# Kernel optimization log

Measured on AMD Instinct MI355X. Metric: run time of the kernel, lower is better.

The kernel has to match this reference:

```python
import jax, jax.numpy as jnp
import numpy as np

N_NODES = 50000
N_EDGES = 1000000
D = 64
L = 3
BN_EPS = 1e-5


def setup_inputs() -> dict:
    key = jax.random.key(0)
    ks = jax.random.split(key, 6)
    x = jax.random.normal(ks[0], (N_NODES, D), dtype=jnp.float32)
    edge_src = jax.random.randint(ks[1], (N_EDGES,), 0, N_NODES)
    edge_dst = jax.random.randint(ks[2], (N_EDGES,), 0, N_NODES)
    edge_weight = jax.random.uniform(ks[3], (N_EDGES,), dtype=jnp.float32)
    W = jax.random.normal(ks[4], (L, D, D), dtype=jnp.float32) * (1.0 / np.sqrt(D))
    b = jnp.zeros((L, D), dtype=jnp.float32)
    prelu_a = jnp.full((L,), 0.25, dtype=jnp.float32)  # torch PReLU default init
    bn_gamma = jnp.ones((L, D), dtype=jnp.float32)
    bn_beta = jnp.zeros((L, D), dtype=jnp.float32)
    return {"x": x, "edge_src": edge_src, "edge_dst": edge_dst,
            "edge_weight": edge_weight, "W": W, "b": b, "prelu_a": prelu_a,
            "bn_gamma": bn_gamma, "bn_beta": bn_beta}


def reference(x, edge_src, edge_dst, edge_weight, W, b, prelu_a, bn_gamma, bn_beta):
    n = x.shape[0]
    h = x
    for i in range(L):
        h_in = h
        # GCNConv (normalize=False): aggregate edge_weight * (h @ W)[src] at dst, + bias
        xw = h @ W[i]                                       # [N, D]
        msg = edge_weight[:, None] * xw[edge_src]            # [E, D] gather
        agg = jax.ops.segment_sum(msg, edge_dst, num_segments=n) + b[i]
        # PReLU (single shared parameter per module)
        h = jnp.where(agg >= 0, agg, prelu_a[i] * agg)
        if i > 0:
            h = h + h_in
        # BatchNorm1d, training-mode batch statistics over nodes
        mean = jnp.mean(h, axis=0)
        var = jnp.mean((h - mean) ** 2, axis=0)  # biased variance, as torch BN
        h = bn_gamma[i] * (h - mean) * jax.lax.rsqrt(var + BN_EPS) + bn_beta[i]
        # dropout p=0.0 -> identity
    return h
```

## Files before the change

kernel.cpp:

```cpp
#include <hip/hip_runtime.h>
#include <hip/hip_fp16.h>

#define N_NODES 50000
#define N_EDGES 1000000
#define D 64
#define L 3
#define BN_EPS 1e-5f
#define NB_SCAN ((N_NODES + 255) / 256)
#define AGG_BLOCKS ((N_NODES + 31) / 32)
#define NXCD 8
#define BN_XSTRIDE (L * 2 * D)

__device__ inline int get_xcc() {
    int x;
    asm volatile("s_getreg_b32 %0, hwreg(HW_REG_XCC_ID)" : "=s"(x));
    return x & (NXCD - 1);
}

__device__ inline void bn_affine8(const float* __restrict__ bnsum_l,
                                  const float* __restrict__ gamma,
                                  const float* __restrict__ beta,
                                  int c, float& sc, float& sh) {
    float s1 = 0.f, s2 = 0.f;
#pragma unroll
    for (int x = 0; x < NXCD; x++) {
        s1 += bnsum_l[(size_t)x * BN_XSTRIDE + c];
        s2 += bnsum_l[(size_t)x * BN_XSTRIDE + D + c];
    }
    float mean = s1 * (1.f / N_NODES);
    float var = fmaf(-mean, mean, s2 * (1.f / N_NODES));
    float inv = rsqrtf(var + BN_EPS);
    sc = gamma[c] * inv;
    sh = fmaf(-mean, sc, beta[c]);
}

__device__ inline float unpack_w(unsigned int m) {
    __half_raw hr;
    hr.x = (unsigned short)(m & 0xffffu);
    __half h = *reinterpret_cast<__half*>(&hr);
    return __half2float(h);
}

__device__ inline float2 unpack_x2(unsigned int q) {
    __half2 h2 = *reinterpret_cast<__half2*>(&q);
    return __half22float2(h2);
}

__device__ inline float2 ntload_f2(const float2* p) {
    unsigned long long u = __builtin_nontemporal_load((const unsigned long long*)p);
    float2 r;
    r.x = __uint_as_float((unsigned int)(u & 0xffffffffull));
    r.y = __uint_as_float((unsigned int)(u >> 32));
    return r;
}

__device__ inline void ntstore_f2(float2* p, float2 v) {
    unsigned long long u =
        ((unsigned long long)__float_as_uint(v.y) << 32) | (unsigned long long)__float_as_uint(v.x);
    __builtin_nontemporal_store(u, (unsigned long long*)p);
}

__global__ void init_kernel(int* __restrict__ counts8, float* __restrict__ bnsum8) {
    int i = blockIdx.x * blockDim.x + threadIdx.x;
    int stride = gridDim.x * blockDim.x;
    for (int j = i; j < NXCD * N_NODES; j += stride) counts8[j] = 0;
    for (int j = i; j < NXCD * BN_XSTRIDE; j += stride) bnsum8[j] = 0.f;
}

__global__ void count_kernel(const int* __restrict__ dst, int* __restrict__ counts8,
                             unsigned short* __restrict__ rankx) {
    int xcd = get_xcc();
    int* mycnt = counts8 + (size_t)xcd * N_NODES;
    int i = blockIdx.x * blockDim.x + threadIdx.x;
    int stride = gridDim.x * blockDim.x;
    for (int e = i; e < N_EDGES; e += stride) {
        int r = atomicAdd(&mycnt[dst[e]], 1);
        rankx[e] = (unsigned short)(r | (xcd << 13));
    }
}

__global__ __launch_bounds__(256) void scanA_kernel(const int* __restrict__ counts8,
                                                    int* __restrict__ counts,
                                                    int* __restrict__ blocksum) {
    __shared__ int buf[256];
    int t = threadIdx.x, b = blockIdx.x;
    int i = b * 256 + t;
    int v = 0;
    if (i < N_NODES) {
#pragma unroll
        for (int x = 0; x < NXCD; x++) v += counts8[(size_t)x * N_NODES + i];
        counts[i] = v;
    }
    buf[t] = v;
    __syncthreads();
    for (int off = 128; off > 0; off >>= 1) {
        if (t < off) buf[t] += buf[t + off];
        __syncthreads();
    }
    if (t == 0) blocksum[b] = buf[0];
}

__global__ __launch_bounds__(256) void scanB_kernel(const int* __restrict__ blocksum,
                                                    int* __restrict__ blockoff,
                                                    int* __restrict__ row_ptr) {
    __shared__ int buf[256];
    int t = threadIdx.x;
    int v = (t < NB_SCAN) ? blocksum[t] : 0;
    buf[t] = v;
    __syncthreads();
    for (int off = 1; off < 256; off <<= 1) {
        int u = (t >= off) ? buf[t - off] : 0;
        __syncthreads();
        buf[t] += u;
        __syncthreads();
    }
    if (t < NB_SCAN) blockoff[t] = buf[t] - v;
    if (t == NB_SCAN - 1) row_ptr[N_NODES] = buf[t];
}

__global__ __launch_bounds__(256) void scanC_kernel(const int* __restrict__ counts,
                                                    const int* __restrict__ counts8,
                                                    const int* __restrict__ blockoff,
                                                    int* __restrict__ row_ptr,
                                                    int* __restrict__ offs8) {
    __shared__ int buf[256];
    int t = threadIdx.x, b = blockIdx.x;
    int i = b * 256 + t;
    int v = (i < N_NODES) ? counts[i] : 0;
    buf[t] = v;
    __syncthreads();
    for (int off = 1; off < 256; off <<= 1) {
        int u = (t >= off) ? buf[t - off] : 0;
        __syncthreads();
        buf[t] += u;
        __syncthreads();
    }
    if (i < N_NODES) {
        int base = blockoff[b] + buf[t] - v;
        row_ptr[i] = base;
#pragma unroll
        for (int x = 0; x < NXCD; x++) {
            offs8[(size_t)x * N_NODES + i] = base;
            base += counts8[(size_t)x * N_NODES + i];
        }
    }
}

__global__ void fill_kernel(const int* __restrict__ src, const int* __restrict__ dst,
                            const float* __restrict__ w,
                            const unsigned short* __restrict__ rankx,
                            const int* __restrict__ offs8,
                            unsigned int* __restrict__ em) {
    int i = blockIdx.x * blockDim.x + threadIdx.x;
    int stride = gridDim.x * blockDim.x;
    for (int e = i; e < N_EDGES; e += stride) {
        int d = dst[e];
        unsigned rx = rankx[e];
        int p = offs8[(size_t)(rx >> 13) * N_NODES + d] + (int)(rx & 0x1fffu);
        __half h = __float2half_rn(w[e]);
        unsigned short wb = reinterpret_cast<__half_raw*>(&h)->x;
        em[p] = ((unsigned int)src[e] << 16) | (unsigned int)wb;
    }
}

__global__ __launch_bounds__(256) void gemm_kernel(const float* __restrict__ hraw,
                                                   const float* __restrict__ bnsum_p,
                                                   const float* __restrict__ gamma_p,
                                                   const float* __restrict__ beta_p,
                                                   const float* __restrict__ Wl,
                                                   __half* __restrict__ xw) {
    __shared__ float aff[2][D];
    int tid = threadIdx.x, lane = tid & 63, wave = tid >> 6;
    if (tid < D) {
        float sc = 1.f, sh = 0.f;
        if (bnsum_p) bn_affine8(bnsum_p, gamma_p, beta_p, tid, sc, sh);
        aff[0][tid] = sc;
        aff[1][tid] = sh;
    }
    __syncthreads();
    float Wreg[D];
    float biasc = 0.f;
#pragma unroll
    for (int k = 0; k < D; k++) {
        float wkc = Wl[k * D + lane];
        biasc = fmaf(aff[1][k], wkc, biasc);
        Wreg[k] = wkc * aff[0][k];
    }
    int gw = blockIdx.x * 4 + wave, nw = gridDim.x * 4;
    for (int v = gw; v < N_NODES; v += nw) {
        const float* hp = hraw + (size_t)__builtin_amdgcn_readfirstlane(v) * D;
        float acc = biasc;
#pragma unroll
        for (int k = 0; k < D; k++) acc = fmaf(hp[k], Wreg[k], acc);
        xw[v * D + lane] = __float2half_rn(acc);
    }
}

__global__ __launch_bounds__(256) void agg_kernel(const uint2* __restrict__ xw,
                                                  const int* __restrict__ row_ptr,
                                                  const unsigned int* __restrict__ em,
                                                  const float* __restrict__ bl,
                                                  const float* __restrict__ pa,
                                                  const float* __restrict__ hraw_prev,
                                                  const float* __restrict__ bnsum_p,
                                                  const float* __restrict__ gamma_p,
                                                  const float* __restrict__ beta_p,
                                                  float* __restrict__ hpre,
                                                  float* __restrict__ bnsum_l) {
    __shared__ float r1[D], r2[D];
    int tid = threadIdx.x, lane = tid & 63;
    int sub = tid >> 4;
    int fl = lane & 15;
    int srcbase = lane & 48;
    if (tid < D) { r1[tid] = 0.f; r2[tid] = 0.f; }
    __syncthreads();

    float al = pa[0];
    int c0 = 4 * fl;
    float4 bias = ((const float4*)bl)[fl];
    float sc0 = 0, sc1 = 0, sc2 = 0, sc3 = 0, sh0 = 0, sh1 = 0, sh2 = 0, sh3 = 0;
    if (hraw_prev) {
        bn_affine8(bnsum_p, gamma_p, beta_p, c0 + 0, sc0, sh0);
        bn_affine8(bnsum_p, gamma_p, beta_p, c0 + 1, sc1, sh1);
        bn_affine8(bnsum_p, gamma_p, beta_p, c0 + 2, sc2, sh2);
        bn_affine8(bnsum_p, gamma_p, beta_p, c0 + 3, sc3, sh3);
    }
    float t1_0 = 0, t1_1 = 0, t1_2 = 0, t1_3 = 0;
    float t2_0 = 0, t2_1 = 0, t2_2 = 0, t2_3 = 0;

    int v0 = (blockIdx.x * 16 + sub) * 2;
    if (v0 < N_NODES) {
        int2 e01 = *(const int2*)(row_ptr + v0);
        int e0 = e01.x, m = e01.y;
        int e2 = row_ptr[v0 + 2];
        float A0 = 0, A1 = 0, A2 = 0, A3 = 0, B0 = 0, B1 = 0, B2 = 0, B3 = 0;
        unsigned mo = (e0 + fl < e2) ? __builtin_nontemporal_load(em + e0 + fl) : 0u;
        for (int e = e0; e < e2; e += 16) {
            unsigned mo_nx =
                (e + 16 + fl < e2) ? __builtin_nontemporal_load(em + e + 16 + fl) : 0u;
            unsigned mj[16];
            uint2 q[16];
#pragma unroll
            for (int j = 0; j < 16; j++) {
                mj[j] = (unsigned)__shfl((int)mo, srcbase + j, 64);
                q[j] = xw[(mj[j] >> 16) * 16 + fl];
            }
#pragma unroll
            for (int j = 0; j < 16; j++) {
                float w = unpack_w(mj[j]);
                bool isB = (e + j) >= m;
                float wa = isB ? 0.f : w;
                float wb = isB ? w : 0.f;
                float2 f01 = unpack_x2(q[j].x);
                float2 f23 = unpack_x2(q[j].y);
                A0 = fmaf(wa, f01.x, A0); A1 = fmaf(wa, f01.y, A1);
                A2 = fmaf(wa, f23.x, A2); A3 = fmaf(wa, f23.y, A3);
                B0 = fmaf(wb, f01.x, B0); B1 = fmaf(wb, f01.y, B1);
                B2 = fmaf(wb, f23.x, B2); B3 = fmaf(wb, f23.y, B3);
            }
            mo = mo_nx;
        }
#pragma unroll
        for (int n = 0; n < 2; n++) {
            int v = v0 + n;
            float h0 = (n ? B0 : A0) + bias.x;
            float h1 = (n ? B1 : A1) + bias.y;
            float h2 = (n ? B2 : A2) + bias.z;
            float h3 = (n ? B3 : A3) + bias.w;
            h0 = h0 >= 0.f ? h0 : al * h0;
            h1 = h1 >= 0.f ? h1 : al * h1;
            h2 = h2 >= 0.f ? h2 : al * h2;
            h3 = h3 >= 0.f ? h3 : al * h3;
            if (hraw_prev) {
                float2 p01 = ntload_f2((const float2*)hraw_prev + v * 32 + 2 * fl);
                float2 p23 = ntload_f2((const float2*)hraw_prev + v * 32 + 2 * fl + 1);
                h0 = fmaf(p01.x, sc0, h0 + sh0);
                h1 = fmaf(p01.y, sc1, h1 + sh1);
                h2 = fmaf(p23.x, sc2, h2 + sh2);
                h3 = fmaf(p23.y, sc3, h3 + sh3);
            }
            ntstore_f2((float2*)hpre + v * 32 + 2 * fl, make_float2(h0, h1));
            ntstore_f2((float2*)hpre + v * 32 + 2 * fl + 1, make_float2(h2, h3));
            t1_0 += h0; t1_1 += h1; t1_2 += h2; t1_3 += h3;
            t2_0 = fmaf(h0, h0, t2_0);
            t2_1 = fmaf(h1, h1, t2_1);
            t2_2 = fmaf(h2, h2, t2_2);
            t2_3 = fmaf(h3, h3, t2_3);
        }
    }
    t1_0 += __shfl_xor(t1_0, 16, 64); t1_0 += __shfl_xor(t1_0, 32, 64);
    t1_1 += __shfl_xor(t1_1, 16, 64); t1_1 += __shfl_xor(t1_1, 32, 64);
    t1_2 += __shfl_xor(t1_2, 16, 64); t1_2 += __shfl_xor(t1_2, 32, 64);
    t1_3 += __shfl_xor(t1_3, 16, 64); t1_3 += __shfl_xor(t1_3, 32, 64);
    t2_0 += __shfl_xor(t2_0, 16, 64); t2_0 += __shfl_xor(t2_0, 32, 64);
    t2_1 += __shfl_xor(t2_1, 16, 64); t2_1 += __shfl_xor(t2_1, 32, 64);
    t2_2 += __shfl_xor(t2_2, 16, 64); t2_2 += __shfl_xor(t2_2, 32, 64);
    t2_3 += __shfl_xor(t2_3, 16, 64); t2_3 += __shfl_xor(t2_3, 32, 64);
    if (lane < 16) {
        atomicAdd(&r1[c0 + 0], t1_0);
        atomicAdd(&r1[c0 + 1], t1_1);
        atomicAdd(&r1[c0 + 2], t1_2);
        atomicAdd(&r1[c0 + 3], t1_3);
        atomicAdd(&r2[c0 + 0], t2_0);
        atomicAdd(&r2[c0 + 1], t2_1);
        atomicAdd(&r2[c0 + 2], t2_2);
        atomicAdd(&r2[c0 + 3], t2_3);
    }
    __syncthreads();
    if (tid < D) {
        float* myb = bnsum_l + (size_t)get_xcc() * BN_XSTRIDE;
        atomicAdd(&myb[tid], r1[tid]);
        atomicAdd(&myb[D + tid], r2[tid]);
    }
}

__global__ __launch_bounds__(256) void bnapply_kernel(const float* __restrict__ hpre,
                                                      const float* __restrict__ bnsum_p,
                                                      const float* __restrict__ gamma_p,
                                                      const float* __restrict__ beta_p,
                                                      float* __restrict__ out) {
    __shared__ float aff[2][D];
    int tid = threadIdx.x;
    if (tid < D) {
        float sc, sh;
        bn_affine8(bnsum_p, gamma_p, beta_p, tid, sc, sh);
        aff[0][tid] = sc;
        aff[1][tid] = sh;
    }
    __syncthreads();
    int i = blockIdx.x * blockDim.x + tid;
    int stride = gridDim.x * blockDim.x;
    const int NQ = N_NODES * D / 4;
    for (int j = i; j < NQ; j += stride) {
        float4 hv = ((const float4*)hpre)[j];
        int c = (j * 4) & 63;
        float4 o;
        o.x = fmaf(hv.x, aff[0][c + 0], aff[1][c + 0]);
        o.y = fmaf(hv.y, aff[0][c + 1], aff[1][c + 1]);
        o.z = fmaf(hv.z, aff[0][c + 2], aff[1][c + 2]);
        o.w = fmaf(hv.w, aff[0][c + 3], aff[1][c + 3]);
        ((float4*)out)[j] = o;
    }
}

extern "C" void kernel_launch(void* const* d_in, const int* in_sizes, int n_in,
                              void* d_out, int out_size, void* d_ws, size_t ws_size,
                              hipStream_t stream) {
    const float* x     = (const float*)d_in[0];
    const int*   esrc  = (const int*)d_in[1];
    const int*   edst  = (const int*)d_in[2];
    const float* ew    = (const float*)d_in[3];
    const float* W     = (const float*)d_in[4];
    const float* b     = (const float*)d_in[5];
    const float* pa    = (const float*)d_in[6];
    const float* gamma = (const float*)d_in[7];
    const float* beta  = (const float*)d_in[8];
    float* out = (float*)d_out;

    char* ws = (char*)d_ws;
    size_t off = 0;
    auto alloc = [&](size_t bytes) -> char* {
        char* p = ws + off;
        off = (off + bytes + 255) & ~(size_t)255;
        return p;
    };
    int*            counts8  = (int*)alloc((size_t)NXCD * N_NODES * 4);
    int*            counts   = (int*)alloc((size_t)N_NODES * 4);
    int*            row_ptr  = (int*)alloc((size_t)(N_NODES + 1) * 4);
    int*            offs8    = (int*)alloc((size_t)NXCD * N_NODES * 4);
    int*            blocksum = (int*)alloc((size_t)NB_SCAN * 4);
    int*            blockoff = (int*)alloc((size_t)NB_SCAN * 4);
    unsigned short* rankx    = (unsigned short*)alloc((size_t)N_EDGES * 2);
    unsigned int*   em       = (unsigned int*)alloc((size_t)N_EDGES * 4);
    __half*         xw       = (__half*)alloc((size_t)N_NODES * D * 2);
    float*          hpre1    = (float*)alloc((size_t)N_NODES * D * 4);
    float*          bnsum8   = (float*)alloc((size_t)NXCD * BN_XSTRIDE * 4);

    init_kernel<<<512, 256, 0, stream>>>(counts8, bnsum8);
    count_kernel<<<2048, 256, 0, stream>>>(edst, counts8, rankx);
    scanA_kernel<<<NB_SCAN, 256, 0, stream>>>(counts8, counts, blocksum);
    scanB_kernel<<<1, 256, 0, stream>>>(blocksum, blockoff, row_ptr);
    scanC_kernel<<<NB_SCAN, 256, 0, stream>>>(counts, counts8, blockoff, row_ptr, offs8);
    fill_kernel<<<2048, 256, 0, stream>>>(esrc, edst, ew, rankx, offs8, em);

    float* hbuf[L] = {out, hpre1, out};
    for (int i = 0; i < L; i++) {
        const float* hin = (i == 0) ? x : hbuf[i - 1];
        const float* bns = (i == 0) ? nullptr : bnsum8 + (i - 1) * 2 * D;
        const float* gmp = (i == 0) ? nullptr : gamma + (i - 1) * D;
        const float* btp = (i == 0) ? nullptr : beta + (i - 1) * D;
        gemm_kernel<<<1024, 256, 0, stream>>>(hin, bns, gmp, btp, W + (size_t)i * D * D, xw);
        agg_kernel<<<AGG_BLOCKS, 256, 0, stream>>>((const uint2*)xw, row_ptr, em,
                                                   b + i * D, pa + i,
                                                   (i == 0) ? nullptr : hbuf[i - 1],
                                                   bns, gmp, btp,
                                                   hbuf[i], bnsum8 + i * 2 * D);
    }
    bnapply_kernel<<<2048, 256, 0, stream>>>(hbuf[2], bnsum8 + 2 * 2 * D,
                                             gamma + 2 * D, beta + 2 * D, out);
}
```

Before: 227.6 us.

## Split feature dimension into two planar halves and aggregate each half separately

The GEMM now writes its fp16 output as two planar half-width tables, each holding 32 features per node. The aggregation kernel is launched twice per layer, once per feature half, so each random gather reads from a table half the previous size. The aim is to make the gathered table fit better in each XCD's L2 and raise its hit rate. In exchange, the edge list and row pointers are read twice per layer, there are twice as many launches, and each per-lane gather is narrower.

```diff
diff --git a/kernel.cpp b/kernel.cpp
--- a/kernel.cpp
+++ b/kernel.cpp
@@ -168,7 +168,7 @@
                                                    const float* __restrict__ gamma_p,
                                                    const float* __restrict__ beta_p,
                                                    const float* __restrict__ Wl,
-                                                   __half* __restrict__ xw) {
+                                                   __half* __restrict__ xw2) {
     __shared__ float aff[2][D];
     int tid = threadIdx.x, lane = tid & 63, wave = tid >> 6;
     if (tid < D) {
@@ -186,17 +186,19 @@
         biasc = fmaf(aff[1][k], wkc, biasc);
         Wreg[k] = wkc * aff[0][k];
     }
+    int halfid = lane >> 5, fl2 = lane & 31;
+    __half* dstp = xw2 + (size_t)halfid * N_NODES * 32;
     int gw = blockIdx.x * 4 + wave, nw = gridDim.x * 4;
     for (int v = gw; v < N_NODES; v += nw) {
         const float* hp = hraw + (size_t)__builtin_amdgcn_readfirstlane(v) * D;
         float acc = biasc;
 #pragma unroll
         for (int k = 0; k < D; k++) acc = fmaf(hp[k], Wreg[k], acc);
-        xw[v * D + lane] = __float2half_rn(acc);
-    }
-}
-
-__global__ __launch_bounds__(256) void agg_kernel(const uint2* __restrict__ xw,
+        dstp[v * 32 + fl2] = __float2half_rn(acc);
+    }
+}
+
+__global__ __launch_bounds__(256) void agg_kernel(const unsigned int* __restrict__ xwh,
                                                   const int* __restrict__ row_ptr,
                                                   const unsigned int* __restrict__ em,
                                                   const float* __restrict__ bl,
@@ -206,44 +208,42 @@
                                                   const float* __restrict__ gamma_p,
                                                   const float* __restrict__ beta_p,
                                                   float* __restrict__ hpre,
-                                                  float* __restrict__ bnsum_l) {
-    __shared__ float r1[D], r2[D];
+                                                  float* __restrict__ bnsum_l,
+                                                  int FH) {
+    __shared__ float r1[32], r2[32];
     int tid = threadIdx.x, lane = tid & 63;
     int sub = tid >> 4;
     int fl = lane & 15;
     int srcbase = lane & 48;
-    if (tid < D) { r1[tid] = 0.f; r2[tid] = 0.f; }
+    if (tid < 32) { r1[tid] = 0.f; r2[tid] = 0.f; }
     __syncthreads();
 
     float al = pa[0];
-    int c0 = 4 * fl;
-    float4 bias = ((const float4*)bl)[fl];
-    float sc0 = 0, sc1 = 0, sc2 = 0, sc3 = 0, sh0 = 0, sh1 = 0, sh2 = 0, sh3 = 0;
+    int c0 = FH * 32 + 2 * fl;
+    float2 bias = ((const float2*)bl)[FH * 16 + fl];
+    float sc0 = 0, sc1 = 0, sh0 = 0, sh1 = 0;
     if (hraw_prev) {
         bn_affine8(bnsum_p, gamma_p, beta_p, c0 + 0, sc0, sh0);
         bn_affine8(bnsum_p, gamma_p, beta_p, c0 + 1, sc1, sh1);
-        bn_affine8(bnsum_p, gamma_p, beta_p, c0 + 2, sc2, sh2);
-        bn_affine8(bnsum_p, gamma_p, beta_p, c0 + 3, sc3, sh3);
-    }
-    float t1_0 = 0, t1_1 = 0, t1_2 = 0, t1_3 = 0;
-    float t2_0 = 0, t2_1 = 0, t2_2 = 0, t2_3 = 0;
+    }
+    float t1_0 = 0, t1_1 = 0, t2_0 = 0, t2_1 = 0;
 
     int v0 = (blockIdx.x * 16 + sub) * 2;
     if (v0 < N_NODES) {
         int2 e01 = *(const int2*)(row_ptr + v0);
         int e0 = e01.x, m = e01.y;
         int e2 = row_ptr[v0 + 2];
-        float A0 = 0, A1 = 0, A2 = 0, A3 = 0, B0 = 0, B1 = 0, B2 = 0, B3 = 0;
+        float A0 = 0, A1 = 0, B0 = 0, B1 = 0;
         unsigned mo = (e0 + fl < e2) ? __builtin_nontemporal_load(em + e0 + fl) : 0u;
         for (int e = e0; e < e2; e += 16) {
             unsigned mo_nx =
                 (e + 16 + fl < e2) ? __builtin_nontemporal_load(em + e + 16 + fl) : 0u;
             unsigned mj[16];
-            uint2 q[16];
+            unsigned q[16];
 #pragma unroll
             for (int j = 0; j < 16; j++) {
                 mj[j] = (unsigned)__shfl((int)mo, srcbase + j, 64);
-                q[j] = xw[(mj[j] >> 16) * 16 + fl];
+                q[j] = xwh[(mj[j] >> 16) * 16 + fl];
             }
 #pragma unroll
             for (int j = 0; j < 16; j++) {
@@ -251,12 +251,9 @@
                 bool isB = (e + j) >= m;
                 float wa = isB ? 0.f : w;
                 float wb = isB ? w : 0.f;
-                float2 f01 = unpack_x2(q[j].x);
-                float2 f23 = unpack_x2(q[j].y);
-                A0 = fmaf(wa, f01.x, A0); A1 = fmaf(wa, f01.y, A1);
-                A2 = fmaf(wa, f23.x, A2); A3 = fmaf(wa, f23.y, A3);
-                B0 = fmaf(wb, f01.x, B0); B1 = fmaf(wb, f01.y, B1);
-                B2 = fmaf(wb, f23.x, B2); B3 = fmaf(wb, f23.y, B3);
+                float2 f = unpack_x2(q[j]);
+                A0 = fmaf(wa, f.x, A0); A1 = fmaf(wa, f.y, A1);
+                B0 = fmaf(wb, f.x, B0); B1 = fmaf(wb, f.y, B1);
             }
             mo = mo_nx;
         }
@@ -265,52 +262,34 @@
             int v = v0 + n;
             float h0 = (n ? B0 : A0) + bias.x;
             float h1 = (n ? B1 : A1) + bias.y;
-            float h2 = (n ? B2 : A2) + bias.z;
-            float h3 = (n ? B3 : A3) + bias.w;
             h0 = h0 >= 0.f ? h0 : al * h0;
             h1 = h1 >= 0.f ? h1 : al * h1;
-            h2 = h2 >= 0.f ? h2 : al * h2;
-            h3 = h3 >= 0.f ? h3 : al * h3;
             if (hraw_prev) {
-                float2 p01 = ntload_f2((const float2*)hraw_prev + v * 32 + 2 * fl);
-                float2 p23 = ntload_f2((const float2*)hraw_prev + v * 32 + 2 * fl + 1);
+                float2 p01 = ntload_f2((const float2*)hraw_prev + v * 32 + FH * 16 + fl);
                 h0 = fmaf(p01.x, sc0, h0 + sh0);
                 h1 = fmaf(p01.y, sc1, h1 + sh1);
-                h2 = fmaf(p23.x, sc2, h2 + sh2);
-                h3 = fmaf(p23.y, sc3, h3 + sh3);
             }
-            ntstore_f2((float2*)hpre + v * 32 + 2 * fl, make_float2(h0, h1));
-            ntstore_f2((float2*)hpre + v * 32 + 2 * fl + 1, make_float2(h2, h3));
-            t1_0 += h0; t1_1 += h1; t1_2 += h2; t1_3 += h3;
+            ntstore_f2((float2*)hpre + v * 32 + FH * 16 + fl, make_float2(h0, h1));
+            t1_0 += h0; t1_1 += h1;
             t2_0 = fmaf(h0, h0, t2_0);
             t2_1 = fmaf(h1, h1, t2_1);
-            t2_2 = fmaf(h2, h2, t2_2);
-            t2_3 = fmaf(h3, h3, t2_3);
         }
     }
     t1_0 += __shfl_xor(t1_0, 16, 64); t1_0 += __shfl_xor(t1_0, 32, 64);
     t1_1 += __shfl_xor(t1_1, 16, 64); t1_1 += __shfl_xor(t1_1, 32, 64);
-    t1_2 += __shfl_xor(t1_2, 16, 64); t1_2 += __shfl_xor(t1_2, 32, 64);
-    t1_3 += __shfl_xor(t1_3, 16, 64); t1_3 += __shfl_xor(t1_3, 32, 64);
     t2_0 += __shfl_xor(t2_0, 16, 64); t2_0 += __shfl_xor(t2_0, 32, 64);
     t2_1 += __shfl_xor(t2_1, 16, 64); t2_1 += __shfl_xor(t2_1, 32, 64);
-    t2_2 += __shfl_xor(t2_2, 16, 64); t2_2 += __shfl_xor(t2_2, 32, 64);
-    t2_3 += __shfl_xor(t2_3, 16, 64); t2_3 += __shfl_xor(t2_3, 32, 64);
     if (lane < 16) {
-        atomicAdd(&r1[c0 + 0], t1_0);
-        atomicAdd(&r1[c0 + 1], t1_1);
-        atomicAdd(&r1[c0 + 2], t1_2);
-        atomicAdd(&r1[c0 + 3], t1_3);
-        atomicAdd(&r2[c0 + 0], t2_0);
-        atomicAdd(&r2[c0 + 1], t2_1);
-        atomicAdd(&r2[c0 + 2], t2_2);
-        atomicAdd(&r2[c0 + 3], t2_3);
-    }
-    __syncthreads();
-    if (tid < D) {
+        atomicAdd(&r1[2 * fl + 0], t1_0);
+        atomicAdd(&r1[2 * fl + 1], t1_1);
+        atomicAdd(&r2[2 * fl + 0], t2_0);
+        atomicAdd(&r2[2 * fl + 1], t2_1);
+    }
+    __syncthreads();
+    if (tid < 32) {
         float* myb = bnsum_l + (size_t)get_xcc() * BN_XSTRIDE;
-        atomicAdd(&myb[tid], r1[tid]);
-        atomicAdd(&myb[D + tid], r2[tid]);
+        atomicAdd(&myb[FH * 32 + tid], r1[tid]);
+        atomicAdd(&myb[D + FH * 32 + tid], r2[tid]);
     }
 }
 
@@ -372,7 +351,7 @@
     int*            blockoff = (int*)alloc((size_t)NB_SCAN * 4);
     unsigned short* rankx    = (unsigned short*)alloc((size_t)N_EDGES * 2);
     unsigned int*   em       = (unsigned int*)alloc((size_t)N_EDGES * 4);
-    __half*         xw       = (__half*)alloc((size_t)N_NODES * D * 2);
+    __half*         xw2      = (__half*)alloc((size_t)2 * N_NODES * 32 * 2);
     float*          hpre1    = (float*)alloc((size_t)N_NODES * D * 4);
     float*          bnsum8   = (float*)alloc((size_t)NXCD * BN_XSTRIDE * 4);
 
@@ -389,12 +368,16 @@
         const float* bns = (i == 0) ? nullptr : bnsum8 + (i - 1) * 2 * D;
         const float* gmp = (i == 0) ? nullptr : gamma + (i - 1) * D;
         const float* btp = (i == 0) ? nullptr : beta + (i - 1) * D;
-        gemm_kernel<<<1024, 256, 0, stream>>>(hin, bns, gmp, btp, W + (size_t)i * D * D, xw);
-        agg_kernel<<<AGG_BLOCKS, 256, 0, stream>>>((const uint2*)xw, row_ptr, em,
-                                                   b + i * D, pa + i,
-                                                   (i == 0) ? nullptr : hbuf[i - 1],
-                                                   bns, gmp, btp,
-                                                   hbuf[i], bnsum8 + i * 2 * D);
+        gemm_kernel<<<1024, 256, 0, stream>>>(hin, bns, gmp, btp, W + (size_t)i * D * D, xw2);
+        for (int FH = 0; FH < 2; FH++) {
+            const unsigned int* xwh =
+                (const unsigned int*)xw2 + (size_t)FH * N_NODES * 16;
+            agg_kernel<<<AGG_BLOCKS, 256, 0, stream>>>(xwh, row_ptr, em,
+                                                       b + i * D, pa + i,
+                                                       (i == 0) ? nullptr : hbuf[i - 1],
+                                                       bns, gmp, btp,
+                                                       hbuf[i], bnsum8 + i * 2 * D, FH);
+        }
     }
     bnapply_kernel<<<2048, 256, 0, stream>>>(hbuf[2], bnsum8 + 2 * 2 * D,
                                              gamma + 2 * D, beta + 2 * D, out);
```

New measurement: 265.1 us. 16.5% more time.
